# Kernel tuning notes

Measured on AMD Instinct MI355X. Metric: run time of the kernel, lower is better.

The kernel has to match this reference:

```python
import jax, jax.numpy as jnp
import numpy as np


def _build_cayley(metric):
    """Cayley table for the Clifford algebra with diagonal metric.
    Blades are indexed by bitmask (0=scalar, 1=e1, 2=e2, 3=e12, 4=e3, ...).
    cayley[i, j, k] = coefficient of blade j in the geometric product e_i * e_k.
    """
    n = len(metric)
    dim = 1 << n
    c = np.zeros((dim, dim, dim), dtype=np.float32)
    for a in range(dim):
        for b in range(dim):
            sign = 1.0
            tmp = a >> 1
            while tmp:  # count basis-vector swaps needed to sort e_a e_b
                if bin(tmp & b).count('1') & 1:
                    sign = -sign
                tmp >>= 1
            common = a & b
            for i in range(n):  # contract repeated basis vectors via the metric
                if common & (1 << i):
                    sign *= metric[i]
            c[a, a ^ b, b] = sign
    return c


def fast_einsum(q_einsum, cayley, k_einsum):
    # geometric product of two multivectors (same einsum as the torch.jit version)
    return jnp.einsum('...i,ijk,...k->...j', q_einsum, cayley, k_einsum)


def _embed_grade1(x, mv_dim):
    # embed a 3D vector as a grade-1 multivector: components at blade bitmasks 1, 2, 4
    mv = jnp.zeros(x.shape[:-1] + (mv_dim,), x.dtype)
    mv = mv.at[..., 1].set(x[..., 0])
    mv = mv.at[..., 2].set(x[..., 1])
    mv = mv.at[..., 4].set(x[..., 2])
    return mv


def setup_inputs() -> dict:
    key = jax.random.key(0)
    k1, k2 = jax.random.split(key)
    B, P, D = 4, 8192, 3
    return {
        'source_cloud': jax.random.normal(k1, (B, P, D), dtype=jnp.float32),
        'target_cloud': jax.random.normal(k2, (B, P, D), dtype=jnp.float32),
        'cayley': jnp.asarray(_build_cayley([1.0, 1.0, 1.0])),  # (8,8,8)
    }


def reference(source_cloud, target_cloud, cayley):
    # KNN (K=1) via full pairwise squared distances: (B, P1, P2)
    d2 = (jnp.sum(source_cloud * source_cloud, -1)[:, :, None]
          + jnp.sum(target_cloud * target_cloud, -1)[:, None, :]
          - 2.0 * jnp.einsum('bid,bjd->bij', source_cloud, target_cloud))
    idx = jnp.argmin(d2, axis=2)  # (B, P1) nearest-neighbor indices (non-differentiable)
    # knn_gather: nn[b, i] = target_cloud[b, idx[b, i]]
    nn = jnp.take_along_axis(target_cloud, idx[..., None], axis=1)  # (B, P1, 3)
    # multivector residual and geometric product with itself via the Cayley table
    diff_mv = _embed_grade1(source_cloud - nn, cayley.shape[0])  # (B, P1, 8)
    gp = fast_einsum(diff_mv, cayley, diff_mv)  # (B, P1, 8)
    # scalar part of v*v equals ||v||^2 under the Euclidean metric
    per_point = gp[..., 0]
    per_cloud = jnp.sum(per_point, axis=1)  # point_reduction='sum'
    return jnp.mean(per_cloud)  # batch_reduction='mean'
```

## Files before the change

kernel.cpp:

```cpp
#include <hip/hip_runtime.h>

#define BATCH 4
#define NPTS 8192
#define NTOT (BATCH * NPTS)

constexpr int THREADS    = 256;
constexpr int SRC_CHUNK  = 1024;
constexpr int TGT_CHUNK  = 512;
constexpr int S_PER_THR  = SRC_CHUNK / THREADS;

constexpr int R1_BLOCKS  = 64;

__device__ __forceinline__ unsigned flipf(float x) {
    unsigned u = __float_as_uint(x);
    return (u & 0x80000000u) ? ~u : (u | 0x80000000u);
}
__device__ __forceinline__ float unflipf(unsigned u) {
    u = (u & 0x80000000u) ? (u & 0x7FFFFFFFu) : ~u;
    return __uint_as_float(u);
}

__global__ __launch_bounds__(256) void init_ws_kernel(unsigned* __restrict__ ws) {
    int i = blockIdx.x * blockDim.x + threadIdx.x;
    if (i < NTOT) ws[i] = 0xFFFFFFFFu;
}

__global__ __launch_bounds__(THREADS) void knn_min_kernel(
        const float* __restrict__ src,
        const float* __restrict__ tgt,
        unsigned* __restrict__ ws)
{
    constexpr int NSC = NPTS / SRC_CHUNK;
    constexpr int NTC = NPTS / TGT_CHUNK;
    int bid = blockIdx.x;
    int tc  = bid % NTC;
    int sc  = (bid / NTC) % NSC;
    int b   = bid / (NTC * NSC);

    __shared__ float4 tsh[TGT_CHUNK];

    const float* tbase = tgt + ((size_t)b * NPTS + (size_t)tc * TGT_CHUNK) * 3;
    for (int k = threadIdx.x; k < TGT_CHUNK; k += THREADS) {
        float x = tbase[3 * k + 0];
        float y = tbase[3 * k + 1];
        float z = tbase[3 * k + 2];
        tsh[k] = make_float4(x, y, z, 0.5f * (x * x + y * y + z * z));
    }

    const float* sbase = src + ((size_t)b * NPTS + (size_t)sc * SRC_CHUNK) * 3;
    float sx[S_PER_THR], sy[S_PER_THR], sz[S_PER_THR], mb[S_PER_THR];
    #pragma unroll
    for (int s = 0; s < S_PER_THR; ++s) {
        int i = threadIdx.x + s * THREADS;
        sx[s] = sbase[3 * i + 0];
        sy[s] = sbase[3 * i + 1];
        sz[s] = sbase[3 * i + 2];
        mb[s] = INFINITY;
    }
    __syncthreads();

    #pragma unroll 8
    for (int j = 0; j < TGT_CHUNK; ++j) {
        float4 t = tsh[j];
        #pragma unroll
        for (int s = 0; s < S_PER_THR; ++s) {
            float m = fmaf(-sx[s], t.x, fmaf(-sy[s], t.y, fmaf(-sz[s], t.z, t.w)));
            mb[s] = fminf(mb[s], m);
        }
    }

    #pragma unroll
    for (int s = 0; s < S_PER_THR; ++s) {
        int i = sc * SRC_CHUNK + threadIdx.x + s * THREADS;
        float hs = 0.5f * (sx[s] * sx[s] + sy[s] * sy[s] + sz[s] * sz[s]);
        atomicMin(&ws[(size_t)b * NPTS + i], flipf(mb[s] + hs));
    }
}

__global__ __launch_bounds__(256) void reduce1_kernel(
        const unsigned* __restrict__ ws,
        float* __restrict__ partials)
{
    __shared__ float acc[256];
    int base = blockIdx.x * (NTOT / R1_BLOCKS);
    float a = unflipf(ws[base + threadIdx.x]) + unflipf(ws[base + threadIdx.x + 256]);
    acc[threadIdx.x] = a;
    __syncthreads();
    for (int off = 128; off > 0; off >>= 1) {
        if (threadIdx.x < off) acc[threadIdx.x] += acc[threadIdx.x + off];
        __syncthreads();
    }
    if (threadIdx.x == 0) partials[blockIdx.x] = acc[0];
}

__global__ __launch_bounds__(64) void reduce2_kernel(
        const float* __restrict__ partials,
        float* __restrict__ out)
{
    float v = partials[threadIdx.x];
    #pragma unroll
    for (int off = 32; off > 0; off >>= 1)
        v += __shfl_down(v, off, 64);
    if (threadIdx.x == 0) out[0] = v * 0.5f;
}

extern "C" void kernel_launch(void* const* d_in, const int* in_sizes, int n_in,
                              void* d_out, int out_size, void* d_ws, size_t ws_size,
                              hipStream_t stream) {
    const float* src = (const float*)d_in[0];
    const float* tgt = (const float*)d_in[1];
    float* out = (float*)d_out;
    unsigned* ws  = (unsigned*)d_ws;
    float* partials = (float*)((char*)d_ws + NTOT * sizeof(unsigned));

    init_ws_kernel<<<(NTOT + 255) / 256, 256, 0, stream>>>(ws);

    constexpr int NSC = NPTS / SRC_CHUNK;
    constexpr int NTC = NPTS / TGT_CHUNK;
    knn_min_kernel<<<BATCH * NSC * NTC, THREADS, 0, stream>>>(src, tgt, ws);

    reduce1_kernel<<<R1_BLOCKS, 256, 0, stream>>>(ws, partials);
    reduce2_kernel<<<1, 64, 0, stream>>>(partials, out);
}
```

Measured before the change: 34.58 us.

## Replace atomicMin workspace with per-tile partial minima reduced in reduce kernel

Removes the init kernel and the global atomicMin on order-flipped floats. Each block now writes its per-source minima into a separate slice indexed by target chunk, and reduce1 takes the min across 32 slices before summing. Tiles also change to 8 sources per thread and 256-target chunks, and the inner loop now handles two targets per iteration. In exchange the workspace grows 32x, reduce1 reads 32x more data, and more source registers per thread may lower occupancy.

```diff
diff --git a/kernel.cpp b/kernel.cpp
--- a/kernel.cpp
+++ b/kernel.cpp
@@ -4,34 +4,19 @@
 #define NPTS 8192
 #define NTOT (BATCH * NPTS)
 
-constexpr int THREADS    = 256;
-constexpr int SRC_CHUNK  = 1024;
-constexpr int TGT_CHUNK  = 512;
-constexpr int S_PER_THR  = SRC_CHUNK / THREADS;
+constexpr int THREADS   = 256;
+constexpr int S_PER_THR = 8;
+constexpr int SRC_CHUNK = THREADS * S_PER_THR;
+constexpr int NSC       = NPTS / SRC_CHUNK;
+constexpr int TGT_CHUNK = 256;
+constexpr int NTC       = NPTS / TGT_CHUNK;
+constexpr int R1_BLOCKS = 64;
 
-constexpr int R1_BLOCKS  = 64;
-
-__device__ __forceinline__ unsigned flipf(float x) {
-    unsigned u = __float_as_uint(x);
-    return (u & 0x80000000u) ? ~u : (u | 0x80000000u);
-}
-__device__ __forceinline__ float unflipf(unsigned u) {
-    u = (u & 0x80000000u) ? (u & 0x7FFFFFFFu) : ~u;
-    return __uint_as_float(u);
-}
-
-__global__ __launch_bounds__(256) void init_ws_kernel(unsigned* __restrict__ ws) {
-    int i = blockIdx.x * blockDim.x + threadIdx.x;
-    if (i < NTOT) ws[i] = 0xFFFFFFFFu;
-}
-
-__global__ __launch_bounds__(THREADS) void knn_min_kernel(
+__global__ __launch_bounds__(THREADS) void knn_partial_kernel(
         const float* __restrict__ src,
         const float* __restrict__ tgt,
-        unsigned* __restrict__ ws)
+        float* __restrict__ ws)
 {
-    constexpr int NSC = NPTS / SRC_CHUNK;
-    constexpr int NTC = NPTS / TGT_CHUNK;
     int bid = blockIdx.x;
     int tc  = bid % NTC;
     int sc  = (bid / NTC) % NSC;
@@ -39,8 +24,9 @@
 
     __shared__ float4 tsh[TGT_CHUNK];
 
-    const float* tbase = tgt + ((size_t)b * NPTS + (size_t)tc * TGT_CHUNK) * 3;
-    for (int k = threadIdx.x; k < TGT_CHUNK; k += THREADS) {
+    {
+        const float* tbase = tgt + ((size_t)b * NPTS + (size_t)tc * TGT_CHUNK) * 3;
+        int k = threadIdx.x;
         float x = tbase[3 * k + 0];
         float y = tbase[3 * k + 1];
         float z = tbase[3 * k + 2];
@@ -59,31 +45,42 @@
     }
     __syncthreads();
 
-    #pragma unroll 8
-    for (int j = 0; j < TGT_CHUNK; ++j) {
-        float4 t = tsh[j];
+    #pragma unroll 4
+    for (int j = 0; j < TGT_CHUNK; j += 2) {
+        float4 t0 = tsh[j];
+        float4 t1 = tsh[j + 1];
         #pragma unroll
         for (int s = 0; s < S_PER_THR; ++s) {
-            float m = fmaf(-sx[s], t.x, fmaf(-sy[s], t.y, fmaf(-sz[s], t.z, t.w)));
-            mb[s] = fminf(mb[s], m);
+            float m0 = fmaf(-sx[s], t0.x, fmaf(-sy[s], t0.y, fmaf(-sz[s], t0.z, t0.w)));
+            float m1 = fmaf(-sx[s], t1.x, fmaf(-sy[s], t1.y, fmaf(-sz[s], t1.z, t1.w)));
+            mb[s] = fminf(mb[s], fminf(m0, m1));
         }
     }
 
+    float* wbase = ws + (size_t)tc * NTOT + (size_t)b * NPTS + (size_t)sc * SRC_CHUNK;
     #pragma unroll
     for (int s = 0; s < S_PER_THR; ++s) {
-        int i = sc * SRC_CHUNK + threadIdx.x + s * THREADS;
         float hs = 0.5f * (sx[s] * sx[s] + sy[s] * sy[s] + sz[s] * sz[s]);
-        atomicMin(&ws[(size_t)b * NPTS + i], flipf(mb[s] + hs));
+        wbase[threadIdx.x + s * THREADS] = mb[s] + hs;
     }
 }
 
 __global__ __launch_bounds__(256) void reduce1_kernel(
-        const unsigned* __restrict__ ws,
+        const float* __restrict__ ws,
         float* __restrict__ partials)
 {
     __shared__ float acc[256];
     int base = blockIdx.x * (NTOT / R1_BLOCKS);
-    float a = unflipf(ws[base + threadIdx.x]) + unflipf(ws[base + threadIdx.x + 256]);
+    float a = 0.0f;
+    #pragma unroll
+    for (int p = 0; p < 2; ++p) {
+        int i = base + threadIdx.x + p * 256;
+        float m = INFINITY;
+        #pragma unroll
+        for (int sl = 0; sl < NTC; ++sl)
+            m = fminf(m, ws[(size_t)sl * NTOT + i]);
+        a += m;
+    }
     acc[threadIdx.x] = a;
     __syncthreads();
     for (int off = 128; off > 0; off >>= 1) {
@@ -110,15 +107,10 @@
     const float* src = (const float*)d_in[0];
     const float* tgt = (const float*)d_in[1];
     float* out = (float*)d_out;
-    unsigned* ws  = (unsigned*)d_ws;
-    float* partials = (float*)((char*)d_ws + NTOT * sizeof(unsigned));
+    float* ws  = (float*)d_ws;
+    float* partials = (float*)((char*)d_ws + (size_t)NTC * NTOT * sizeof(float));
 
-    init_ws_kernel<<<(NTOT + 255) / 256, 256, 0, stream>>>(ws);
-
-    constexpr int NSC = NPTS / SRC_CHUNK;
-    constexpr int NTC = NPTS / TGT_CHUNK;
-    knn_min_kernel<<<BATCH * NSC * NTC, THREADS, 0, stream>>>(src, tgt, ws);
-
+    knn_partial_kernel<<<BATCH * NSC * NTC, THREADS, 0, stream>>>(src, tgt, ws);
     reduce1_kernel<<<R1_BLOCKS, 256, 0, stream>>>(ws, partials);
     reduce2_kernel<<<1, 64, 0, stream>>>(partials, out);
 }
```

Result: faster. 33.17 us (-4.1%).
